# Kernel tuning notes

Measured on AMD Instinct MI355X. Metric: run time of the kernel, lower is better.

The kernel has to match this reference:

```python
import jax, jax.numpy as jnp
import numpy as np

SPATIAL = ((92, 92), (46, 46), (23, 23), (12, 12))
N_LEVELS, N_HEADS, N_POINTS = 4, 8, 4
D_MODEL, D_FFN = 256, 1024
D_HEAD = D_MODEL // N_HEADS
LEVEL_SIZES = [h * w for h, w in SPATIAL]
N_TOTAL = sum(LEVEL_SIZES)
B = 4


def _layer_norm(x, g, b, eps=1e-5):
    m = jnp.mean(x, -1, keepdims=True)
    v = jnp.mean((x - m) ** 2, -1, keepdims=True)
    return (x - m) * jax.lax.rsqrt(v + eps) * g + b


def _ref_points_level(H, W, vr, corr):
    # vr: [B,2] (x,y valid ratios); corr: [B,HW,1]
    yy, xx = jnp.meshgrid(jnp.arange(H, dtype=jnp.float32) + 0.5,
                          jnp.arange(W, dtype=jnp.float32) + 0.5, indexing='ij')
    ref = jnp.stack([xx.reshape(-1), yy.reshape(-1)], -1)  # [HW,2] (x,y)
    ref = ref[None] / (vr[:, None, :] * jnp.array([W, H], jnp.float32))  # [B,HW,2]
    # masked_fill(corr < 0.5, -inf) then softmax over dim=1 (safe: all-masked -> zeros)
    logits = jnp.where(corr < 0.5, -jnp.inf, corr)  # [B,HW,1]
    mx = jnp.max(logits, axis=1, keepdims=True)
    mx = jnp.where(jnp.isfinite(mx), mx, 0.0)
    e = jnp.where(jnp.isfinite(logits), jnp.exp(logits - mx), 0.0)
    den = jnp.sum(e, axis=1, keepdims=True)
    sm = jnp.where(den > 0, e / jnp.maximum(den, 1e-30), 0.0)
    center = jnp.einsum('bnc,bnd->bcd', sm, ref)  # [B,1,2] weighted center
    delta = jnp.clip(center - ref, -0.5, 0.5) * sm
    return ref + delta


def _bilinear_sample(v, loc, H, W):
    # v: [B,heads,HW,d]; loc: [B,heads,Q,2] normalized to [0,1]
    # matches F.grid_sample(align_corners=False, padding_mode='zeros')
    x = loc[..., 0] * W - 0.5
    y = loc[..., 1] * H - 0.5
    x0 = jnp.floor(x)
    y0 = jnp.floor(y)
    wx = (x - x0)[..., None]
    wy = (y - y0)[..., None]
    x0i = x0.astype(jnp.int32)
    y0i = y0.astype(jnp.int32)

    def g(yi, xi):
        valid = ((xi >= 0) & (xi < W) & (yi >= 0) & (yi < H)).astype(v.dtype)[..., None]
        idx = jnp.clip(yi, 0, H - 1) * W + jnp.clip(xi, 0, W - 1)
        return jnp.take_along_axis(v, idx[..., None], axis=2) * valid

    top = g(y0i, x0i) * (1 - wx) + g(y0i, x0i + 1) * wx
    bot = g(y0i + 1, x0i) * (1 - wx) + g(y0i + 1, x0i + 1) * wx
    return top * (1 - wy) + bot * wy


def setup_inputs() -> dict:
    key = jax.random.key(0)
    ks = jax.random.split(key, 24)
    f32 = jnp.float32
    s = 0.02
    inp = {}
    inp['src'] = jax.random.normal(ks[0], (B, N_TOTAL, D_MODEL), f32)
    inp['pos'] = jax.random.normal(ks[1], (B, N_TOTAL, D_MODEL), f32)
    for i, sz in enumerate(LEVEL_SIZES):
        inp['corr%d' % i] = jax.random.uniform(ks[2 + i], (B, sz, 1), f32)
    inp['valid_ratios'] = jnp.ones((B, N_LEVELS, 2), f32)
    inp['padding_mask'] = jnp.zeros((B, N_TOTAL), bool)
    dq = D_MODEL + 1  # query concatenated with correlation channel
    inp['W_off'] = jax.random.normal(ks[6], (dq, N_HEADS * N_LEVELS * N_POINTS * 2), f32) * s
    inp['b_off'] = jax.random.normal(ks[7], (N_HEADS * N_LEVELS * N_POINTS * 2,), f32) * s
    inp['W_attn'] = jax.random.normal(ks[8], (dq, N_HEADS * N_LEVELS * N_POINTS), f32) * s
    inp['b_attn'] = jax.random.normal(ks[9], (N_HEADS * N_LEVELS * N_POINTS,), f32) * s
    inp['W_val'] = jax.random.normal(ks[10], (D_MODEL, D_MODEL), f32) * s
    inp['b_val'] = jax.random.normal(ks[11], (D_MODEL,), f32) * s
    inp['W_out'] = jax.random.normal(ks[12], (D_MODEL, D_MODEL), f32) * s
    inp['b_out'] = jax.random.normal(ks[13], (D_MODEL,), f32) * s
    inp['ln1_g'] = jnp.ones((D_MODEL,), f32)
    inp['ln1_b'] = jnp.zeros((D_MODEL,), f32)
    inp['W1'] = jax.random.normal(ks[14], (D_MODEL, D_FFN), f32) * s
    inp['b1'] = jax.random.normal(ks[15], (D_FFN,), f32) * s
    inp['W2'] = jax.random.normal(ks[16], (D_FFN, D_MODEL), f32) * s
    inp['b2'] = jax.random.normal(ks[17], (D_MODEL,), f32) * s
    inp['ln2_g'] = jnp.ones((D_MODEL,), f32)
    inp['ln2_b'] = jnp.zeros((D_MODEL,), f32)
    return inp


def reference(src, pos, corr0, corr1, corr2, corr3, valid_ratios, padding_mask,
              W_off, b_off, W_attn, b_attn, W_val, b_val, W_out, b_out,
              ln1_g, ln1_b, W1, b1, W2, b2, ln2_g, ln2_b):
    corr_maps = (corr0, corr1, corr2, corr3)
    refs = [_ref_points_level(H, W, valid_ratios[:, l], corr_maps[l])
            for l, (H, W) in enumerate(SPATIAL)]
    ref = jnp.concatenate(refs, axis=1)                      # [B,N,2]
    reference_points = ref[:, :, None, :] * valid_ratios[:, None]  # [B,N,L,2]
    query = jnp.concatenate([src + pos, jnp.concatenate(corr_maps, 1)], -1)  # [B,N,257]

    # --- MSDeformAttn ---
    value = jnp.where(padding_mask[..., None], 0.0, src @ W_val + b_val)
    value = value.reshape(B, N_TOTAL, N_HEADS, D_HEAD)
    offsets = (query @ W_off + b_off).reshape(B, N_TOTAL, N_HEADS, N_LEVELS, N_POINTS, 2)
    attn = jax.nn.softmax((query @ W_attn + b_attn)
                          .reshape(B, N_TOTAL, N_HEADS, N_LEVELS * N_POINTS), -1)
    attn = attn.reshape(B, N_TOTAL, N_HEADS, N_LEVELS, N_POINTS)
    normalizer = jnp.array([[w, h] for h, w in SPATIAL], jnp.float32)  # [L,2] (W,H)
    loc = reference_points[:, :, None, :, None, :] + \
        offsets / normalizer[None, None, None, :, None, :]  # [B,N,h,L,P,2]

    out = jnp.zeros((B, N_TOTAL, N_HEADS, D_HEAD), src.dtype)
    start = 0
    for l, (H, W) in enumerate(SPATIAL):
        sz = H * W
        v = value[:, start:start + sz].transpose(0, 2, 1, 3)  # [B,h,HW,d]
        ll = loc[:, :, :, l].transpose(0, 2, 1, 3, 4).reshape(B, N_HEADS, N_TOTAL * N_POINTS, 2)
        s = _bilinear_sample(v, ll, H, W).reshape(B, N_HEADS, N_TOTAL, N_POINTS, D_HEAD)
        w = attn[:, :, :, l].transpose(0, 2, 1, 3)            # [B,h,N,P]
        out = out + jnp.einsum('bhnpd,bhnp->bnhd', s, w)
        start += sz
    src2 = out.reshape(B, N_TOTAL, D_MODEL) @ W_out + b_out

    x = _layer_norm(src + src2, ln1_g, ln1_b)
    ff = jax.nn.relu(x @ W1 + b1) @ W2 + b2
    return _layer_norm(x + ff, ln2_g, ln2_b)
```

## Files before the change

### kernel.cpp

```cpp
#include <hip/hip_runtime.h>

#define MT 45012
#define NTOT 11253
#define BB 4

typedef __attribute__((ext_vector_type(8))) __bf16 bf16x8;
typedef __attribute__((ext_vector_type(4))) float f32x4;

__device__ __forceinline__ unsigned short f2bf(float f) {
  unsigned u = __float_as_uint(f);
  u += 0x7FFFu + ((u >> 16) & 1u);
  return (unsigned short)(u >> 16);
}

__global__ __launch_bounds__(256) void wt_transpose(const float* __restrict__ W,
                                                    unsigned short* __restrict__ Wt,
                                                    int K, int N) {
  int i = blockIdx.x * 256 + threadIdx.x;
  if (i >= K * N) return;
  int n = i / K, k = i % K;
  Wt[i] = f2bf(W[(size_t)k * N + n]);
}

__global__ __launch_bounds__(256) void cvec_kernel(const float* __restrict__ Woff,
                                                   const float* __restrict__ Wattn,
                                                   float* __restrict__ c_off,
                                                   float* __restrict__ c_attn) {
  int i = blockIdx.x * 256 + threadIdx.x;
  if (i < 256) c_off[i] = Woff[256 * 256 + i];
  else if (i < 384) c_attn[i - 256] = Wattn[256 * 128 + (i - 256)];
}

__global__ __launch_bounds__(256) void cvt_kernel(const float4* __restrict__ src4,
                                                  const float4* __restrict__ pos4,
                                                  ushort4* __restrict__ sb,
                                                  ushort4* __restrict__ qb) {
  int i = blockIdx.x * 256 + threadIdx.x;
  if (i >= MT * 64) return;
  float4 s = src4[i], p = pos4[i];
  sb[i] = make_ushort4(f2bf(s.x), f2bf(s.y), f2bf(s.z), f2bf(s.w));
  qb[i] = make_ushort4(f2bf(s.x + p.x), f2bf(s.y + p.y), f2bf(s.z + p.z), f2bf(s.w + p.w));
}

__global__ __launch_bounds__(256) void stats_kernel(const float* __restrict__ c0,
                                                    const float* __restrict__ c1,
                                                    const float* __restrict__ c2,
                                                    const float* __restrict__ c3,
                                                    const float* __restrict__ vr,
                                                    float* __restrict__ stats) {
  const int LS[4] = {92, 46, 23, 12};
  const int LHW[4] = {8464, 2116, 529, 144};
  int b = blockIdx.x >> 2, l = blockIdx.x & 3;
  const float* cp = (l == 0) ? c0 : (l == 1) ? c1 : (l == 2) ? c2 : c3;
  int S = LS[l], HW = LHW[l];
  float vrx = vr[(b * 4 + l) * 2 + 0], vry = vr[(b * 4 + l) * 2 + 1];
  int tid = threadIdx.x;
  __shared__ float red[4];

  float mx = -INFINITY;
  for (int i = tid; i < HW; i += 256) {
    float c = cp[(size_t)b * HW + i];
    if (c >= 0.5f) mx = fmaxf(mx, c);
  }
  for (int o = 32; o; o >>= 1) mx = fmaxf(mx, __shfl_xor(mx, o));
  if ((tid & 63) == 0) red[tid >> 6] = mx;
  __syncthreads();
  mx = fmaxf(fmaxf(red[0], red[1]), fmaxf(red[2], red[3]));
  float mx_eff = isinf(mx) ? 0.f : mx;
  __syncthreads();

  float den = 0.f, cx = 0.f, cy = 0.f;
  float invW = 1.f / (vrx * (float)S), invH = 1.f / (vry * (float)S);
  for (int i = tid; i < HW; i += 256) {
    float c = cp[(size_t)b * HW + i];
    if (c >= 0.5f) {
      float e = expf(c - mx_eff);
      int x = i % S, y = i / S;
      den += e;
      cx += e * ((float)x + 0.5f) * invW;
      cy += e * ((float)y + 0.5f) * invH;
    }
  }
  float vals[3] = {den, cx, cy};
  for (int j = 0; j < 3; ++j) {
    float v = vals[j];
    for (int o = 32; o; o >>= 1) v += __shfl_xor(v, o);
    if ((tid & 63) == 0) red[tid >> 6] = v;
    __syncthreads();
    v = red[0] + red[1] + red[2] + red[3];
    vals[j] = v;
    __syncthreads();
  }
  if (tid == 0) {
    float* s = stats + (size_t)(b * 4 + l) * 4;
    s[0] = mx_eff; s[1] = vals[0]; s[2] = vals[1]; s[3] = vals[2];
  }
}

__global__ __launch_bounds__(256) void refpt_kernel(const float* __restrict__ c0,
                                                    const float* __restrict__ c1,
                                                    const float* __restrict__ c2,
                                                    const float* __restrict__ c3,
                                                    const float* __restrict__ vr,
                                                    const float* __restrict__ stats,
                                                    float* __restrict__ refpt,
                                                    float* __restrict__ corr_all) {
  int i = blockIdx.x * 256 + threadIdx.x;
  if (i >= MT) return;
  int b = i / NTOT, n = i % NTOT;
  int l = (n < 8464) ? 0 : (n < 10580) ? 1 : (n < 11109) ? 2 : 3;
  const int LS[4] = {92, 46, 23, 12};
  const int LSTART[4] = {0, 8464, 10580, 11109};
  const int LHW[4] = {8464, 2116, 529, 144};
  int S = LS[l], start = LSTART[l], HW = LHW[l];
  int local = n - start;
  int x = local % S, y = local / S;
  float vrx = vr[(b * 4 + l) * 2 + 0], vry = vr[(b * 4 + l) * 2 + 1];
  float rx = ((float)x + 0.5f) / (vrx * (float)S);
  float ry = ((float)y + 0.5f) / (vry * (float)S);
  const float* cp = (l == 0) ? c0 : (l == 1) ? c1 : (l == 2) ? c2 : c3;
  float c = cp[(size_t)b * HW + local];
  const float* st = stats + (size_t)(b * 4 + l) * 4;
  float mx = st[0], den = st[1], cxs = st[2], cys = st[3];
  float sm = 0.f, cenx = 0.f, ceny = 0.f;
  if (den > 0.f) {
    if (c >= 0.5f) sm = expf(c - mx) / fmaxf(den, 1e-30f);
    cenx = cxs / den; ceny = cys / den;
  }
  float dx = fminf(fmaxf(cenx - rx, -0.5f), 0.5f) * sm;
  float dy = fminf(fmaxf(ceny - ry, -0.5f), 0.5f) * sm;
  refpt[2 * i] = rx + dx;
  refpt[2 * i + 1] = ry + dy;
  corr_all[i] = c;
}

template <int EPI>
__global__ __launch_bounds__(256) void gemm_bf16(const unsigned short* __restrict__ A,
                                                 const unsigned short* __restrict__ Bt,
                                                 const float* __restrict__ bias,
                                                 const float* __restrict__ cvec,
                                                 const float* __restrict__ corr,
                                                 const float* __restrict__ resid,
                                                 void* __restrict__ out,
                                                 int K, int N) {
  const int tid = threadIdx.x;
  const int wid = tid >> 6, lane = tid & 63;
  const int row0 = blockIdx.x * 64;
  const int col0 = blockIdx.y * 128;
  const int wm = wid >> 1, wn = wid & 1;
  const int l15 = lane & 15, lk = (lane >> 4) * 8;

  __shared__ __align__(16) unsigned short Als[64 * 40];
  __shared__ __align__(16) unsigned short Bls[128 * 40];

  f32x4 acc[2][4];
  const f32x4 zero = {0.f, 0.f, 0.f, 0.f};
#pragma unroll
  for (int a = 0; a < 2; ++a)
#pragma unroll
    for (int c = 0; c < 4; ++c) acc[a][c] = zero;

  const int srow = tid >> 2, sseg = tid & 3;
  for (int k0 = 0; k0 < K; k0 += 32) {
    __syncthreads();
    {
      int grow = row0 + srow;
      uint4 v = make_uint4(0, 0, 0, 0);
      if (grow < MT) v = *(const uint4*)(A + (size_t)grow * K + k0 + sseg * 8);
      *(uint4*)(&Als[srow * 40 + sseg * 8]) = v;
    }
#pragma unroll
    for (int it = 0; it < 2; ++it) {
      int r = srow + it * 64;
      uint4 v = *(const uint4*)(Bt + (size_t)(col0 + r) * K + k0 + sseg * 8);
      *(uint4*)(&Bls[r * 40 + sseg * 8]) = v;
    }
    __syncthreads();
    bf16x8 av[2], bv[4];
#pragma unroll
    for (int fm = 0; fm < 2; ++fm)
      av[fm] = *(const bf16x8*)(&Als[(wm * 32 + fm * 16 + l15) * 40 + lk]);
#pragma unroll
    for (int fn = 0; fn < 4; ++fn)
      bv[fn] = *(const bf16x8*)(&Bls[(wn * 64 + fn * 16 + l15) * 40 + lk]);
#pragma unroll
    for (int fm = 0; fm < 2; ++fm)
#pragma unroll
      for (int fn = 0; fn < 4; ++fn)
        acc[fm][fn] = __builtin_amdgcn_mfma_f32_16x16x32_bf16(av[fm], bv[fn], acc[fm][fn], 0, 0, 0);
  }

#pragma unroll
  for (int fm = 0; fm < 2; ++fm) {
#pragma unroll
    for (int fn = 0; fn < 4; ++fn) {
      int gcol = col0 + wn * 64 + fn * 16 + l15;
      float bcol = bias[gcol];
#pragma unroll
      for (int r = 0; r < 4; ++r) {
        int grow = row0 + wm * 32 + fm * 16 + (lane >> 4) * 4 + r;
        if (grow < MT) {
          float v = acc[fm][fn][r] + bcol;
          if constexpr (EPI == 1) v += corr[grow] * cvec[gcol];
          if constexpr (EPI == 2) v += resid[(size_t)grow * N + gcol];
          if constexpr (EPI == 3) {
            ((unsigned short*)out)[(size_t)grow * N + gcol] = f2bf(fmaxf(v, 0.f));
          } else if constexpr (EPI == 4) {
            ((unsigned short*)out)[(size_t)grow * N + gcol] = f2bf(v);
          } else {
            ((float*)out)[(size_t)grow * N + gcol] = v;
          }
        }
      }
    }
  }
}

__global__ __launch_bounds__(256) void softmax16(float* __restrict__ a) {
  int idx = blockIdx.x * 256 + threadIdx.x;
  if (idx >= MT * 8) return;
  float* p = a + (size_t)idx * 16;
  float4 v0 = ((float4*)p)[0], v1 = ((float4*)p)[1], v2 = ((float4*)p)[2], v3 = ((float4*)p)[3];
  float m = fmaxf(fmaxf(fmaxf(v0.x, v0.y), fmaxf(v0.z, v0.w)),
                  fmaxf(fmaxf(fmaxf(v1.x, v1.y), fmaxf(v1.z, v1.w)),
                        fmaxf(fmaxf(fmaxf(v2.x, v2.y), fmaxf(v2.z, v2.w)),
                              fmaxf(fmaxf(v3.x, v3.y), fmaxf(v3.z, v3.w)))));
  v0.x = expf(v0.x - m); v0.y = expf(v0.y - m); v0.z = expf(v0.z - m); v0.w = expf(v0.w - m);
  v1.x = expf(v1.x - m); v1.y = expf(v1.y - m); v1.z = expf(v1.z - m); v1.w = expf(v1.w - m);
  v2.x = expf(v2.x - m); v2.y = expf(v2.y - m); v2.z = expf(v2.z - m); v2.w = expf(v2.w - m);
  v3.x = expf(v3.x - m); v3.y = expf(v3.y - m); v3.z = expf(v3.z - m); v3.w = expf(v3.w - m);
  float s = v0.x + v0.y + v0.z + v0.w + v1.x + v1.y + v1.z + v1.w +
            v2.x + v2.y + v2.z + v2.w + v3.x + v3.y + v3.z + v3.w;
  float inv = 1.f / s;
  v0.x *= inv; v0.y *= inv; v0.z *= inv; v0.w *= inv;
  v1.x *= inv; v1.y *= inv; v1.z *= inv; v1.w *= inv;
  v2.x *= inv; v2.y *= inv; v2.z *= inv; v2.w *= inv;
  v3.x *= inv; v3.y *= inv; v3.z *= inv; v3.w *= inv;
  ((float4*)p)[0] = v0; ((float4*)p)[1] = v1; ((float4*)p)[2] = v2; ((float4*)p)[3] = v3;
}

__global__ __launch_bounds__(256) void sampler2_kernel(const unsigned short* __restrict__ value,
                                                       const float* __restrict__ offs,
                                                       const float* __restrict__ attw,
                                                       const float* __restrict__ refpt,
                                                       const float* __restrict__ vr,
                                                       unsigned short* __restrict__ outs) {
  const int LS[4] = {92, 46, 23, 12};
  const int LSTART[4] = {0, 8464, 10580, 11109};
  const int tid = threadIdx.x;
  const int rsel = tid >> 7;
  const int r = blockIdx.x * 2 + rsel;

  __shared__ __align__(16) int4 s_addr[2][128];
  __shared__ __align__(16) float4 s_w[2][128];

  {
    int pt = tid & 127;
    int l = (pt >> 2) & 3;
    int h = pt >> 4;
    int b = r / NTOT;
    float ox = offs[(size_t)r * 256 + pt * 2];
    float oy = offs[(size_t)r * 256 + pt * 2 + 1];
    float aw = attw[(size_t)r * 128 + pt];
    float rx = refpt[2 * r], ry = refpt[2 * r + 1];
    float vrx = vr[(b * 4 + l) * 2 + 0], vry = vr[(b * 4 + l) * 2 + 1];
    int S = LS[l];
    float fS = (float)S;
    float xf = rx * vrx * fS + ox - 0.5f;
    float yf = ry * vry * fS + oy - 0.5f;
    float x0f = floorf(xf), y0f = floorf(yf);
    float wx = xf - x0f, wy = yf - y0f;
    int x0 = (int)x0f, y0 = (int)y0f;
    int x1 = x0 + 1, y1 = y0 + 1;
    float vx0 = ((unsigned)x0 < (unsigned)S) ? 1.f : 0.f;
    float vx1 = ((unsigned)x1 < (unsigned)S) ? 1.f : 0.f;
    float vy0 = ((unsigned)y0 < (unsigned)S) ? 1.f : 0.f;
    float vy1 = ((unsigned)y1 < (unsigned)S) ? 1.f : 0.f;
    int cx0 = min(max(x0, 0), S - 1), cx1 = min(max(x1, 0), S - 1);
    int cy0 = min(max(y0, 0), S - 1), cy1 = min(max(y1, 0), S - 1);
    int base = (b * NTOT + LSTART[l]) * 512 + h * 64;
    int4 a;
    a.x = base + (cy0 * S + cx0) * 512;
    a.y = base + (cy0 * S + cx1) * 512;
    a.z = base + (cy1 * S + cx0) * 512;
    a.w = base + (cy1 * S + cx1) * 512;
    float iwx = 1.f - wx, iwy = 1.f - wy;
    float4 w;
    w.x = aw * iwx * iwy * vx0 * vy0;
    w.y = aw * wx * iwy * vx1 * vy0;
    w.z = aw * iwx * wy * vx0 * vy1;
    w.w = aw * wx * wy * vx1 * vy1;
    s_addr[rsel][pt] = a;
    s_w[rsel][pt] = w;
  }
  __syncthreads();

  const int h = (tid >> 4) & 7, cp = tid & 15;
  const char* vb = (const char*)value;
  const int cpo = cp * 4;
  float a0 = 0.f, a1 = 0.f;
#pragma unroll 4
  for (int i = 0; i < 16; ++i) {
    int4 a = s_addr[rsel][h * 16 + i];
    float4 w = s_w[rsel][h * 16 + i];
    unsigned u00 = *(const unsigned*)(vb + (size_t)(unsigned)(a.x + cpo));
    unsigned u01 = *(const unsigned*)(vb + (size_t)(unsigned)(a.y + cpo));
    unsigned u10 = *(const unsigned*)(vb + (size_t)(unsigned)(a.z + cpo));
    unsigned u11 = *(const unsigned*)(vb + (size_t)(unsigned)(a.w + cpo));
    float f00l = __uint_as_float(u00 << 16), f00h = __uint_as_float(u00 & 0xFFFF0000u);
    float f01l = __uint_as_float(u01 << 16), f01h = __uint_as_float(u01 & 0xFFFF0000u);
    float f10l = __uint_as_float(u10 << 16), f10h = __uint_as_float(u10 & 0xFFFF0000u);
    float f11l = __uint_as_float(u11 << 16), f11h = __uint_as_float(u11 & 0xFFFF0000u);
    a0 += w.x * f00l + w.y * f01l + w.z * f10l + w.w * f11l;
    a1 += w.x * f00h + w.y * f01h + w.z * f10h + w.w * f11h;
  }
  unsigned packed = (unsigned)f2bf(a0) | ((unsigned)f2bf(a1) << 16);
  ((unsigned*)outs)[(size_t)r * 128 + h * 16 + cp] = packed;
}

__global__ __launch_bounds__(256) void ln_kernel(const float* __restrict__ in,
                                                 const float* __restrict__ g,
                                                 const float* __restrict__ b,
                                                 float* __restrict__ outf,
                                                 ushort4* __restrict__ outbf) {
  int row = blockIdx.x * 4 + (threadIdx.x >> 6);
  int lane = threadIdx.x & 63;
  if (row >= MT) return;
  const float4* p = (const float4*)(in + (size_t)row * 256);
  float4 v = p[lane];
  float s = v.x + v.y + v.z + v.w;
  for (int o = 32; o; o >>= 1) s += __shfl_xor(s, o);
  float mean = s * (1.f / 256.f);
  float dx = v.x - mean, dy = v.y - mean, dz = v.z - mean, dw = v.w - mean;
  float q = dx * dx + dy * dy + dz * dz + dw * dw;
  for (int o = 32; o; o >>= 1) q += __shfl_xor(q, o);
  float rstd = rsqrtf(q * (1.f / 256.f) + 1e-5f);
  float4 gv = ((const float4*)g)[lane];
  float4 bv = ((const float4*)b)[lane];
  float4 o;
  o.x = dx * rstd * gv.x + bv.x;
  o.y = dy * rstd * gv.y + bv.y;
  o.z = dz * rstd * gv.z + bv.z;
  o.w = dw * rstd * gv.w + bv.w;
  ((float4*)(outf + (size_t)row * 256))[lane] = o;
  if (outbf) outbf[(size_t)row * 64 + lane] = make_ushort4(f2bf(o.x), f2bf(o.y), f2bf(o.z), f2bf(o.w));
}

extern "C" void kernel_launch(void* const* d_in, const int* in_sizes, int n_in,
                              void* d_out, int out_size, void* d_ws, size_t ws_size,
                              hipStream_t stream) {
  (void)in_sizes; (void)n_in; (void)out_size; (void)ws_size;
  const float* src = (const float*)d_in[0];
  const float* pos = (const float*)d_in[1];
  const float* c0 = (const float*)d_in[2];
  const float* c1 = (const float*)d_in[3];
  const float* c2 = (const float*)d_in[4];
  const float* c3 = (const float*)d_in[5];
  const float* vr = (const float*)d_in[6];
  const float* W_off = (const float*)d_in[8];
  const float* b_off = (const float*)d_in[9];
  const float* W_attn = (const float*)d_in[10];
  const float* b_attn = (const float*)d_in[11];
  const float* W_val = (const float*)d_in[12];
  const float* b_val = (const float*)d_in[13];
  const float* W_out = (const float*)d_in[14];
  const float* b_out = (const float*)d_in[15];
  const float* ln1g = (const float*)d_in[16];
  const float* ln1b = (const float*)d_in[17];
  const float* W1 = (const float*)d_in[18];
  const float* b1 = (const float*)d_in[19];
  const float* W2 = (const float*)d_in[20];
  const float* b2 = (const float*)d_in[21];
  const float* ln2g = (const float*)d_in[22];
  const float* ln2b = (const float*)d_in[23];

  char* ws = (char*)d_ws;
  unsigned short* value_bf = (unsigned short*)(ws + 0);
  float* tbuf = (float*)(ws + 0);
  float* xbuf = tbuf;
  float* ubuf = tbuf;
  float* offs = (float*)(ws + 46092288);
  unsigned short* x_bf16 = (unsigned short*)(ws + 46092288);
  unsigned short* src_bf16 = (unsigned short*)(ws + 92184576);
  unsigned short* out_s = src_bf16;
  unsigned short* qa = (unsigned short*)(ws + 115230720);
  float* logits = (float*)(ws + 138276864);
  unsigned short* hbuf = (unsigned short*)(ws + 115230720);
  unsigned short* Wt_val = (unsigned short*)(ws + 207415296);
  unsigned short* Wt_off = (unsigned short*)(ws + 207546368);
  unsigned short* Wt_attn = (unsigned short*)(ws + 207677440);
  unsigned short* Wt_out = (unsigned short*)(ws + 207742976);
  unsigned short* Wt1 = (unsigned short*)(ws + 207874048);
  unsigned short* Wt2 = (unsigned short*)(ws + 208398336);
  float* c_off = (float*)(ws + 208922624);
  float* c_attn = (float*)(ws + 208923648);
  float* refpt = (float*)(ws + 208924160);
  float* corr_all = (float*)(ws + 209284256);
  float* stats = (float*)(ws + 209464304);

  wt_transpose<<<256, 256, 0, stream>>>(W_val, Wt_val, 256, 256);
  wt_transpose<<<256, 256, 0, stream>>>(W_off, Wt_off, 256, 256);
  wt_transpose<<<128, 256, 0, stream>>>(W_attn, Wt_attn, 256, 128);
  wt_transpose<<<256, 256, 0, stream>>>(W_out, Wt_out, 256, 256);
  wt_transpose<<<1024, 256, 0, stream>>>(W1, Wt1, 256, 1024);
  wt_transpose<<<1024, 256, 0, stream>>>(W2, Wt2, 1024, 256);
  cvec_kernel<<<2, 256, 0, stream>>>(W_off, W_attn, c_off, c_attn);

  cvt_kernel<<<11253, 256, 0, stream>>>((const float4*)src, (const float4*)pos,
                                        (ushort4*)src_bf16, (ushort4*)qa);
  stats_kernel<<<16, 256, 0, stream>>>(c0, c1, c2, c3, vr, stats);
  refpt_kernel<<<176, 256, 0, stream>>>(c0, c1, c2, c3, vr, stats, refpt, corr_all);

  dim3 blk(256);
  gemm_bf16<4><<<dim3(704, 2), blk, 0, stream>>>(src_bf16, Wt_val, b_val, nullptr, nullptr, nullptr, value_bf, 256, 256);
  gemm_bf16<1><<<dim3(704, 2), blk, 0, stream>>>(qa, Wt_off, b_off, c_off, corr_all, nullptr, offs, 256, 256);
  gemm_bf16<1><<<dim3(704, 1), blk, 0, stream>>>(qa, Wt_attn, b_attn, c_attn, corr_all, nullptr, logits, 256, 128);
  softmax16<<<1407, 256, 0, stream>>>(logits);
  sampler2_kernel<<<MT / 2, 256, 0, stream>>>(value_bf, offs, logits, refpt, vr, out_s);
  gemm_bf16<2><<<dim3(704, 2), blk, 0, stream>>>(out_s, Wt_out, b_out, nullptr, nullptr, src, tbuf, 256, 256);
  ln_kernel<<<11253, 256, 0, stream>>>(tbuf, ln1g, ln1b, xbuf, (ushort4*)x_bf16);
  gemm_bf16<3><<<dim3(704, 8), blk, 0, stream>>>(x_bf16, Wt1, b1, nullptr, nullptr, nullptr, hbuf, 256, 1024);
  gemm_bf16<2><<<dim3(704, 2), blk, 0, stream>>>(hbuf, Wt2, b2, nullptr, nullptr, xbuf, ubuf, 1024, 256);
  ln_kernel<<<11253, 256, 0, stream>>>(ubuf, ln2g, ln2b, (float*)d_out, nullptr);
}
```

Before: 390.5 us.

## Enlarge GEMM tiles with direct global-to-LDS loads, fuse softmax into sampler, merge prep kernels

The GEMM tile grows from 64x128 to 128x128 so each wave computes a 64x64 block, and tiles are loaded with global_load_lds straight into unpadded LDS. Out-of-range A rows are clamped to the last row, with the epilogue guard still masking the stores. The attention softmax moves into the sampler via 16-lane shuffles, which drops a kernel and a pass over the logits. The six weight transposes and the cvec copy are merged into one launch. The unpadded LDS layout may cause bank conflicts, and the larger tile roughly halves the number of GEMM blocks.

New measurement: 375.2 us. 1.04x faster.

```diff
diff --git a/kernel.cpp b/kernel.cpp
--- a/kernel.cpp
+++ b/kernel.cpp
@@ -13,22 +13,35 @@
   return (unsigned short)(u >> 16);
 }
 
-__global__ __launch_bounds__(256) void wt_transpose(const float* __restrict__ W,
-                                                    unsigned short* __restrict__ Wt,
-                                                    int K, int N) {
-  int i = blockIdx.x * 256 + threadIdx.x;
-  if (i >= K * N) return;
+__device__ __forceinline__ void gld16(const unsigned short* g, unsigned short* l) {
+  __builtin_amdgcn_global_load_lds((const __attribute__((address_space(1))) unsigned int*)g,
+                                   (__attribute__((address_space(3))) unsigned int*)l, 16, 0, 0);
+}
+
+__global__ __launch_bounds__(256) void prep_kernel(const float* __restrict__ Wv, const float* __restrict__ Wo,
+                                                   const float* __restrict__ Wa, const float* __restrict__ Wu,
+                                                   const float* __restrict__ W1, const float* __restrict__ W2,
+                                                   unsigned short* __restrict__ Tv, unsigned short* __restrict__ To,
+                                                   unsigned short* __restrict__ Ta, unsigned short* __restrict__ Tu,
+                                                   unsigned short* __restrict__ T1, unsigned short* __restrict__ T2,
+                                                   float* __restrict__ c_off, float* __restrict__ c_attn) {
+  int bid = blockIdx.x, t = threadIdx.x;
+  const float* W; unsigned short* T; int K, N, base;
+  if (bid < 256)       { W = Wv; T = Tv; K = 256;  N = 256;  base = 0; }
+  else if (bid < 512)  { W = Wo; T = To; K = 256;  N = 256;  base = 256; }
+  else if (bid < 640)  { W = Wa; T = Ta; K = 256;  N = 128;  base = 512; }
+  else if (bid < 896)  { W = Wu; T = Tu; K = 256;  N = 256;  base = 640; }
+  else if (bid < 1920) { W = W1; T = T1; K = 256;  N = 1024; base = 896; }
+  else if (bid < 2944) { W = W2; T = T2; K = 1024; N = 256;  base = 1920; }
+  else {
+    int i = (bid - 2944) * 256 + t;
+    if (i < 256) c_off[i] = Wo[256 * 256 + i];
+    else if (i < 384) c_attn[i - 256] = Wa[256 * 128 + (i - 256)];
+    return;
+  }
+  int i = (bid - base) * 256 + t;
   int n = i / K, k = i % K;
-  Wt[i] = f2bf(W[(size_t)k * N + n]);
-}
-
-__global__ __launch_bounds__(256) void cvec_kernel(const float* __restrict__ Woff,
-                                                   const float* __restrict__ Wattn,
-                                                   float* __restrict__ c_off,
-                                                   float* __restrict__ c_attn) {
-  int i = blockIdx.x * 256 + threadIdx.x;
-  if (i < 256) c_off[i] = Woff[256 * 256 + i];
-  else if (i < 384) c_attn[i - 256] = Wattn[256 * 128 + (i - 256)];
+  T[i] = f2bf(W[(size_t)k * N + n]);
 }
 
 __global__ __launch_bounds__(256) void cvt_kernel(const float4* __restrict__ src4,
@@ -135,73 +148,78 @@
 }
 
 template <int EPI>
-__global__ __launch_bounds__(256) void gemm_bf16(const unsigned short* __restrict__ A,
-                                                 const unsigned short* __restrict__ Bt,
-                                                 const float* __restrict__ bias,
-                                                 const float* __restrict__ cvec,
-                                                 const float* __restrict__ corr,
-                                                 const float* __restrict__ resid,
-                                                 void* __restrict__ out,
-                                                 int K, int N) {
+__global__ __launch_bounds__(256) void gemm128(const unsigned short* __restrict__ A,
+                                               const unsigned short* __restrict__ Bt,
+                                               const float* __restrict__ bias,
+                                               const float* __restrict__ cvec,
+                                               const float* __restrict__ corr,
+                                               const float* __restrict__ resid,
+                                               void* __restrict__ out,
+                                               int K, int N) {
   const int tid = threadIdx.x;
   const int wid = tid >> 6, lane = tid & 63;
-  const int row0 = blockIdx.x * 64;
+  const int row0 = blockIdx.x * 128;
   const int col0 = blockIdx.y * 128;
   const int wm = wid >> 1, wn = wid & 1;
-  const int l15 = lane & 15, lk = (lane >> 4) * 8;
-
-  __shared__ __align__(16) unsigned short Als[64 * 40];
-  __shared__ __align__(16) unsigned short Bls[128 * 40];
-
-  f32x4 acc[2][4];
+  const int l15 = lane & 15;
+  const int hi = lane >> 4;
+
+  __shared__ __align__(16) unsigned short Als[128 * 32];
+  __shared__ __align__(16) unsigned short Bls[128 * 32];
+
+  f32x4 acc[4][4];
   const f32x4 zero = {0.f, 0.f, 0.f, 0.f};
 #pragma unroll
-  for (int a = 0; a < 2; ++a)
+  for (int a = 0; a < 4; ++a)
 #pragma unroll
     for (int c = 0; c < 4; ++c) acc[a][c] = zero;
 
-  const int srow = tid >> 2, sseg = tid & 3;
+  const int i0 = tid, i1 = 256 + tid;
+  int ar0 = row0 + (i0 >> 2); if (ar0 > MT - 1) ar0 = MT - 1;
+  int ar1 = row0 + (i1 >> 2); if (ar1 > MT - 1) ar1 = MT - 1;
+  const unsigned short* ga0 = A + (size_t)ar0 * K + (i0 & 3) * 8;
+  const unsigned short* ga1 = A + (size_t)ar1 * K + (i1 & 3) * 8;
+  const unsigned short* gb0 = Bt + (size_t)(col0 + (i0 >> 2)) * K + (i0 & 3) * 8;
+  const unsigned short* gb1 = Bt + (size_t)(col0 + (i1 >> 2)) * K + (i1 & 3) * 8;
+  unsigned short* la0 = Als + i0 * 8;
+  unsigned short* la1 = Als + i1 * 8;
+  unsigned short* lb0 = Bls + i0 * 8;
+  unsigned short* lb1 = Bls + i1 * 8;
+
   for (int k0 = 0; k0 < K; k0 += 32) {
     __syncthreads();
-    {
-      int grow = row0 + srow;
-      uint4 v = make_uint4(0, 0, 0, 0);
-      if (grow < MT) v = *(const uint4*)(A + (size_t)grow * K + k0 + sseg * 8);
-      *(uint4*)(&Als[srow * 40 + sseg * 8]) = v;
+    gld16(ga0 + k0, la0);
+    gld16(ga1 + k0, la1);
+    gld16(gb0 + k0, lb0);
+    gld16(gb1 + k0, lb1);
+    __syncthreads();
+    bf16x8 av[4], bv[4];
+#pragma unroll
+    for (int f = 0; f < 4; ++f) {
+      av[f] = *(const bf16x8*)(Als + (wm * 64 + f * 16 + l15) * 32 + hi * 8);
+      bv[f] = *(const bf16x8*)(Bls + (wn * 64 + f * 16 + l15) * 32 + hi * 8);
     }
 #pragma unroll
-    for (int it = 0; it < 2; ++it) {
-      int r = srow + it * 64;
-      uint4 v = *(const uint4*)(Bt + (size_t)(col0 + r) * K + k0 + sseg * 8);
-      *(uint4*)(&Bls[r * 40 + sseg * 8]) = v;
-    }
-    __syncthreads();
-    bf16x8 av[2], bv[4];
-#pragma unroll
-    for (int fm = 0; fm < 2; ++fm)
-      av[fm] = *(const bf16x8*)(&Als[(wm * 32 + fm * 16 + l15) * 40 + lk]);
-#pragma unroll
-    for (int fn = 0; fn < 4; ++fn)
-      bv[fn] = *(const bf16x8*)(&Bls[(wn * 64 + fn * 16 + l15) * 40 + lk]);
-#pragma unroll
-    for (int fm = 0; fm < 2; ++fm)
+    for (int fm = 0; fm < 4; ++fm)
 #pragma unroll
       for (int fn = 0; fn < 4; ++fn)
         acc[fm][fn] = __builtin_amdgcn_mfma_f32_16x16x32_bf16(av[fm], bv[fn], acc[fm][fn], 0, 0, 0);
   }
 
 #pragma unroll
-  for (int fm = 0; fm < 2; ++fm) {
+  for (int fm = 0; fm < 4; ++fm) {
 #pragma unroll
     for (int fn = 0; fn < 4; ++fn) {
       int gcol = col0 + wn * 64 + fn * 16 + l15;
       float bcol = bias[gcol];
+      float cv = 0.f;
+      if constexpr (EPI == 1) cv = cvec[gcol];
 #pragma unroll
       for (int r = 0; r < 4; ++r) {
-        int grow = row0 + wm * 32 + fm * 16 + (lane >> 4) * 4 + r;
+        int grow = row0 + wm * 64 + fm * 16 + hi * 4 + r;
         if (grow < MT) {
           float v = acc[fm][fn][r] + bcol;
-          if constexpr (EPI == 1) v += corr[grow] * cvec[gcol];
+          if constexpr (EPI == 1) v += corr[grow] * cv;
           if constexpr (EPI == 2) v += resid[(size_t)grow * N + gcol];
           if constexpr (EPI == 3) {
             ((unsigned short*)out)[(size_t)grow * N + gcol] = f2bf(fmaxf(v, 0.f));
@@ -216,32 +234,9 @@
   }
 }
 
-__global__ __launch_bounds__(256) void softmax16(float* __restrict__ a) {
-  int idx = blockIdx.x * 256 + threadIdx.x;
-  if (idx >= MT * 8) return;
-  float* p = a + (size_t)idx * 16;
-  float4 v0 = ((float4*)p)[0], v1 = ((float4*)p)[1], v2 = ((float4*)p)[2], v3 = ((float4*)p)[3];
-  float m = fmaxf(fmaxf(fmaxf(v0.x, v0.y), fmaxf(v0.z, v0.w)),
-                  fmaxf(fmaxf(fmaxf(v1.x, v1.y), fmaxf(v1.z, v1.w)),
-                        fmaxf(fmaxf(fmaxf(v2.x, v2.y), fmaxf(v2.z, v2.w)),
-                              fmaxf(fmaxf(v3.x, v3.y), fmaxf(v3.z, v3.w)))));
-  v0.x = expf(v0.x - m); v0.y = expf(v0.y - m); v0.z = expf(v0.z - m); v0.w = expf(v0.w - m);
-  v1.x = expf(v1.x - m); v1.y = expf(v1.y - m); v1.z = expf(v1.z - m); v1.w = expf(v1.w - m);
-  v2.x = expf(v2.x - m); v2.y = expf(v2.y - m); v2.z = expf(v2.z - m); v2.w = expf(v2.w - m);
-  v3.x = expf(v3.x - m); v3.y = expf(v3.y - m); v3.z = expf(v3.z - m); v3.w = expf(v3.w - m);
-  float s = v0.x + v0.y + v0.z + v0.w + v1.x + v1.y + v1.z + v1.w +
-            v2.x + v2.y + v2.z + v2.w + v3.x + v3.y + v3.z + v3.w;
-  float inv = 1.f / s;
-  v0.x *= inv; v0.y *= inv; v0.z *= inv; v0.w *= inv;
-  v1.x *= inv; v1.y *= inv; v1.z *= inv; v1.w *= inv;
-  v2.x *= inv; v2.y *= inv; v2.z *= inv; v2.w *= inv;
-  v3.x *= inv; v3.y *= inv; v3.z *= inv; v3.w *= inv;
-  ((float4*)p)[0] = v0; ((float4*)p)[1] = v1; ((float4*)p)[2] = v2; ((float4*)p)[3] = v3;
-}
-
 __global__ __launch_bounds__(256) void sampler2_kernel(const unsigned short* __restrict__ value,
                                                        const float* __restrict__ offs,
-                                                       const float* __restrict__ attw,
+                                                       const float* __restrict__ logits,
                                                        const float* __restrict__ refpt,
                                                        const float* __restrict__ vr,
                                                        unsigned short* __restrict__ outs) {
@@ -251,8 +246,8 @@
   const int rsel = tid >> 7;
   const int r = blockIdx.x * 2 + rsel;
 
-  __shared__ __align__(16) int4 s_addr[2][128];
-  __shared__ __align__(16) float4 s_w[2][128];
+  __shared__ __align__(16) int4 s_addr[2][8][17];
+  __shared__ __align__(16) float4 s_w[2][8][17];
 
   {
     int pt = tid & 127;
@@ -261,7 +256,14 @@
     int b = r / NTOT;
     float ox = offs[(size_t)r * 256 + pt * 2];
     float oy = offs[(size_t)r * 256 + pt * 2 + 1];
-    float aw = attw[(size_t)r * 128 + pt];
+    float lg = logits[(size_t)r * 128 + pt];
+    float m = lg;
+    for (int o = 1; o < 16; o <<= 1) m = fmaxf(m, __shfl_xor(m, o));
+    float e = expf(lg - m);
+    float s = e;
+    for (int o = 1; o < 16; o <<= 1) s += __shfl_xor(s, o);
+    float aw = e / s;
+
     float rx = refpt[2 * r], ry = refpt[2 * r + 1];
     float vrx = vr[(b * 4 + l) * 2 + 0], vry = vr[(b * 4 + l) * 2 + 1];
     int S = LS[l];
@@ -290,8 +292,8 @@
     w.y = aw * wx * iwy * vx1 * vy0;
     w.z = aw * iwx * wy * vx0 * vy1;
     w.w = aw * wx * wy * vx1 * vy1;
-    s_addr[rsel][pt] = a;
-    s_w[rsel][pt] = w;
+    s_addr[rsel][h][pt & 15] = a;
+    s_w[rsel][h][pt & 15] = w;
   }
   __syncthreads();
 
@@ -301,8 +303,8 @@
   float a0 = 0.f, a1 = 0.f;
 #pragma unroll 4
   for (int i = 0; i < 16; ++i) {
-    int4 a = s_addr[rsel][h * 16 + i];
-    float4 w = s_w[rsel][h * 16 + i];
+    int4 a = s_addr[rsel][h][i];
+    float4 w = s_w[rsel][h][i];
     unsigned u00 = *(const unsigned*)(vb + (size_t)(unsigned)(a.x + cpo));
     unsigned u01 = *(const unsigned*)(vb + (size_t)(unsigned)(a.y + cpo));
     unsigned u10 = *(const unsigned*)(vb + (size_t)(unsigned)(a.z + cpo));
@@ -398,13 +400,9 @@
   float* corr_all = (float*)(ws + 209284256);
   float* stats = (float*)(ws + 209464304);
 
-  wt_transpose<<<256, 256, 0, stream>>>(W_val, Wt_val, 256, 256);
-  wt_transpose<<<256, 256, 0, stream>>>(W_off, Wt_off, 256, 256);
-  wt_transpose<<<128, 256, 0, stream>>>(W_attn, Wt_attn, 256, 128);
-  wt_transpose<<<256, 256, 0, stream>>>(W_out, Wt_out, 256, 256);
-  wt_transpose<<<1024, 256, 0, stream>>>(W1, Wt1, 256, 1024);
-  wt_transpose<<<1024, 256, 0, stream>>>(W2, Wt2, 1024, 256);
-  cvec_kernel<<<2, 256, 0, stream>>>(W_off, W_attn, c_off, c_attn);
+  prep_kernel<<<2946, 256, 0, stream>>>(W_val, W_off, W_attn, W_out, W1, W2,
+                                        Wt_val, Wt_off, Wt_attn, Wt_out, Wt1, Wt2,
+                                        c_off, c_attn);
 
   cvt_kernel<<<11253, 256, 0, stream>>>((const float4*)src, (const float4*)pos,
                                         (ushort4*)src_bf16, (ushort4*)qa);
@@ -412,14 +410,13 @@
   refpt_kernel<<<176, 256, 0, stream>>>(c0, c1, c2, c3, vr, stats, refpt, corr_all);
 
   dim3 blk(256);
-  gemm_bf16<4><<<dim3(704, 2), blk, 0, stream>>>(src_bf16, Wt_val, b_val, nullptr, nullptr, nullptr, value_bf, 256, 256);
-  gemm_bf16<1><<<dim3(704, 2), blk, 0, stream>>>(qa, Wt_off, b_off, c_off, corr_all, nullptr, offs, 256, 256);
-  gemm_bf16<1><<<dim3(704, 1), blk, 0, stream>>>(qa, Wt_attn, b_attn, c_attn, corr_all, nullptr, logits, 256, 128);
-  softmax16<<<1407, 256, 0, stream>>>(logits);
+  gemm128<4><<<dim3(352, 2), blk, 0, stream>>>(src_bf16, Wt_val, b_val, nullptr, nullptr, nullptr, value_bf, 256, 256);
+  gemm128<1><<<dim3(352, 2), blk, 0, stream>>>(qa, Wt_off, b_off, c_off, corr_all, nullptr, offs, 256, 256);
+  gemm128<1><<<dim3(352, 1), blk, 0, stream>>>(qa, Wt_attn, b_attn, c_attn, corr_all, nullptr, logits, 256, 128);
   sampler2_kernel<<<MT / 2, 256, 0, stream>>>(value_bf, offs, logits, refpt, vr, out_s);
-  gemm_bf16<2><<<dim3(704, 2), blk, 0, stream>>>(out_s, Wt_out, b_out, nullptr, nullptr, src, tbuf, 256, 256);
+  gemm128<2><<<dim3(352, 2), blk, 0, stream>>>(out_s, Wt_out, b_out, nullptr, nullptr, src, tbuf, 256, 256);
   ln_kernel<<<11253, 256, 0, stream>>>(tbuf, ln1g, ln1b, xbuf, (ushort4*)x_bf16);
-  gemm_bf16<3><<<dim3(704, 8), blk, 0, stream>>>(x_bf16, Wt1, b1, nullptr, nullptr, nullptr, hbuf, 256, 1024);
-  gemm_bf16<2><<<dim3(704, 2), blk, 0, stream>>>(hbuf, Wt2, b2, nullptr, nullptr, xbuf, ubuf, 1024, 256);
+  gemm128<3><<<dim3(352, 8), blk, 0, stream>>>(x_bf16, Wt1, b1, nullptr, nullptr, nullptr, hbuf, 256, 1024);
+  gemm128<2><<<dim3(352, 2), blk, 0, stream>>>(hbuf, Wt2, b2, nullptr, nullptr, xbuf, ubuf, 1024, 256);
   ln_kernel<<<11253, 256, 0, stream>>>(ubuf, ln2g, ln2b, (float*)d_out, nullptr);
 }
```
